# Optimization experiments

Hardware: AMD Instinct MI355X
Metric: run time of the kernel (lower is better)

Reference implementation:

```python
import jax, jax.numpy as jnp
import numpy as np

B, S, D = 4, 2048, 1024
H, HD = 16, 64  # num_heads, head_size
NEG = -1e20


def setup_inputs() -> dict:
    key = jax.random.key(0)
    ks = jax.random.split(key, 8)
    query = jax.random.normal(ks[0], (B, S, D), dtype=jnp.float32)
    k_in = jax.random.normal(ks[1], (B, S, D), dtype=jnp.float32)
    v_in = jax.random.normal(ks[2], (B, S, D), dtype=jnp.float32)
    # causal mask: True where attention is DISALLOWED (masked_fill semantics)
    mask = jnp.triu(jnp.ones((S, S), dtype=bool), k=1)
    scale = 1.0 / np.sqrt(D)
    Wq = jax.random.normal(ks[3], (D, H * HD), dtype=jnp.float32) * scale
    Wk = jax.random.normal(ks[4], (D, H * HD), dtype=jnp.float32) * scale
    Wv = jax.random.normal(ks[5], (D, H * HD), dtype=jnp.float32) * scale
    Wo = jax.random.normal(ks[6], (H * HD, D), dtype=jnp.float32) * scale
    bo = jnp.zeros((D,), dtype=jnp.float32)
    return {"query": query, "key": k_in, "value": v_in, "mask": mask,
            "Wq": Wq, "Wk": Wk, "Wv": Wv, "Wo": Wo, "bo": bo}


def reference(query, key, value, mask, Wq, Wk, Wv, Wo, bo):
    # projections -> [B, H, S, HD]
    q = (query @ Wq).reshape(B, -1, H, HD).transpose(0, 2, 1, 3)
    k = (key @ Wk).reshape(B, -1, H, HD).transpose(0, 2, 1, 3)
    v = (value @ Wv).reshape(B, -1, H, HD).transpose(0, 2, 1, 3)
    # scaled dot-product attention with boolean mask (True = masked out)
    scores = jnp.einsum('bhqd,bhkd->bhqk', q, k) / jnp.sqrt(jnp.float32(HD))
    scores = jnp.where(mask, jnp.float32(NEG), scores)
    attn = jax.nn.softmax(scores, axis=-1)
    out = jnp.einsum('bhqk,bhkd->bhqd', attn, v)  # [B,H,S,HD]
    out = out.transpose(0, 2, 1, 3).reshape(B, -1, H * HD)
    return out @ Wo + bo
```

## Files before the change

### kernel.cpp

```cpp
#include <hip/hip_runtime.h>

#define B_ 4
#define S_ 2048
#define D_ 1024
#define H_ 16
#define HD_ 64

typedef __attribute__((ext_vector_type(8))) short bf16x8;
typedef __attribute__((ext_vector_type(4))) float f32x4;

__device__ __forceinline__ short f2bf(float f) {
  unsigned u = __builtin_bit_cast(unsigned, f);
  u += 0x7fffu + ((u >> 16) & 1u);
  return (short)(u >> 16);
}

__device__ __forceinline__ unsigned cvtpk(float a, float b) {
  unsigned r;
  asm("v_cvt_pk_bf16_f32 %0, %1, %2" : "=v"(r) : "v"(a), "v"(b));
  return r;
}

__device__ __forceinline__ void gload_lds16(const void* g, void* l) {
  __builtin_amdgcn_global_load_lds((const __attribute__((address_space(1))) void*)g,
                                   (__attribute__((address_space(3))) void*)l, 16, 0, 0);
}

__device__ __forceinline__ bf16x8 ldsw8(const short* base, int row, int colb) {
  const int off = (row * 128 + colb) ^ ((row & 7) << 4);
  return *(const bf16x8*)((const char*)base + off);
}

#define MFMA16(a, b, c) __builtin_amdgcn_mfma_f32_16x16x32_bf16((a), (b), (c), 0, 0, 0)

__global__ void cast_f32_bf16(const float* __restrict__ in, short* __restrict__ out, int n4) {
  const int i = blockIdx.x * blockDim.x + threadIdx.x;
  if (i < n4) {
    const float4 f = ((const float4*)in)[i];
    short4 o;
    o.x = f2bf(f.x); o.y = f2bf(f.y); o.z = f2bf(f.z); o.w = f2bf(f.w);
    ((short4*)out)[i] = o;
  }
}

__global__ void transpose_cast_w4(const float* __restrict__ W0, const float* __restrict__ W1,
                                  const float* __restrict__ W2, const float* __restrict__ W3,
                                  short* __restrict__ T0, short* __restrict__ T1,
                                  short* __restrict__ T2, short* __restrict__ T3) {
  __shared__ float tile[32][33];
  const int z = blockIdx.z;
  const float* W = z == 0 ? W0 : z == 1 ? W1 : z == 2 ? W2 : W3;
  short* Wt = z == 0 ? T0 : z == 1 ? T1 : z == 2 ? T2 : T3;
  const int n0 = blockIdx.x * 32, k0 = blockIdx.y * 32;
  const int tx = threadIdx.x, ty = threadIdx.y;
  #pragma unroll
  for (int i = ty; i < 32; i += 8)
    tile[i][tx] = W[(size_t)(k0 + i) * 1024 + n0 + tx];
  __syncthreads();
  #pragma unroll
  for (int i = ty; i < 32; i += 8)
    Wt[(size_t)(n0 + i) * 1024 + k0 + tx] = f2bf(tile[tx][i]);
}

template <int LAYOUT>
__global__ __launch_bounds__(256) void gemm128(const short* __restrict__ A,
                                               const short* __restrict__ Bt,
                                               short* __restrict__ outb,
                                               float* __restrict__ outf,
                                               const float* __restrict__ bias,
                                               float oscale) {
  __shared__ __align__(16) short As[2][128 * 32];
  __shared__ __align__(16) short Bs[2][128 * 32];
  const int tid = threadIdx.x;
  const int l = tid & 63;
  const int w = tid >> 6;
  const int wm = w >> 1, wn = w & 1;
  const int flat = blockIdx.x + (blockIdx.y << 3);
  const int xcd = flat & 7, t = flat >> 3;
  const int row0 = (xcd * 8 + (t & 7)) * 128;
  const int col0 = (t >> 3) * 128;
  const int l15 = l & 15, lq = l >> 4;

  f32x4 acc[4][4] = {};

  auto stage = [&](const short* src, int r0, int k0, short* lds) {
    #pragma unroll
    for (int i = 0; i < 2; i++) {
      int eoff = w * 1024 + i * 512 + l * 8;
      int r = eoff >> 5, kk = eoff & 31;
      gload_lds16(src + (size_t)(r0 + r) * 1024 + k0 + kk, lds + w * 1024 + i * 512);
    }
  };

  stage(A, row0, 0, As[0]);
  stage(Bt, col0, 0, Bs[0]);

  for (int kt = 0; kt < 32; ++kt) {
    __syncthreads();
    if (kt + 1 < 32) {
      stage(A, row0, (kt + 1) * 32, As[(kt + 1) & 1]);
      stage(Bt, col0, (kt + 1) * 32, Bs[(kt + 1) & 1]);
    }
    const short* as = As[kt & 1];
    const short* bs = Bs[kt & 1];
    bf16x8 af[4], bfv[4];
    #pragma unroll
    for (int mf = 0; mf < 4; mf++)
      af[mf] = *(const bf16x8*)(as + (wm * 64 + mf * 16 + l15) * 32 + lq * 8);
    #pragma unroll
    for (int nf = 0; nf < 4; nf++)
      bfv[nf] = *(const bf16x8*)(bs + (wn * 64 + nf * 16 + l15) * 32 + lq * 8);
    #pragma unroll
    for (int mf = 0; mf < 4; mf++)
      #pragma unroll
      for (int nf = 0; nf < 4; nf++)
        acc[mf][nf] = MFMA16(af[mf], bfv[nf], acc[mf][nf]);
  }

  #pragma unroll
  for (int mf = 0; mf < 4; mf++) {
    #pragma unroll
    for (int nf = 0; nf < 4; nf++) {
      #pragma unroll
      for (int r = 0; r < 4; r++) {
        const int gr = row0 + wm * 64 + mf * 16 + lq * 4 + r;
        const int gc = col0 + wn * 64 + nf * 16 + l15;
        const float v = acc[mf][nf][r];
        if (LAYOUT == 0) {
          const int b = gr >> 11, s = gr & 2047;
          const int h = gc >> 6, hd = gc & 63;
          outb[(((size_t)(b * H_ + h)) * S_ + s) * HD_ + hd] = f2bf(v * oscale);
        } else if (LAYOUT == 1) {
          const int b = gr >> 11, s = gr & 2047;
          const int h = gc >> 6, hd = gc & 63;
          outb[(((size_t)(b * H_ + h)) * HD_ + hd) * S_ + s] = f2bf(v);
        } else {
          outf[(size_t)gr * 1024 + gc] = v + bias[gc];
        }
      }
    }
  }
}

__global__ __launch_bounds__(256) void attn_kernel(const short* __restrict__ Qh,
                                                   const short* __restrict__ Kh,
                                                   const short* __restrict__ Vtr,
                                                   short* __restrict__ attnout) {
  __shared__ __align__(16) short Ks[2][64 * 64];
  __shared__ __align__(16) short Vs[2][64 * 64];
  __shared__ __align__(16) short Ps[4][32 * 64];
  const int tid = threadIdx.x, l = tid & 63, w = tid >> 6;
  const int l15 = l & 15, lq = l >> 4;
  const int flat = blockIdx.x;
  const int vid = (flat & 7) * 64 + (flat >> 3);
  const int bh = vid >> 3, pairx = vid & 7;
  const int b = bh >> 4, h = bh & 15;
  const size_t base = (size_t)bh * (S_ * HD_);
  const short* Qp = Qh + base;
  const short* Kp = Kh + base;
  const short* Vp = Vtr + base;
  short* Pw = (short*)Ps[w];

  for (int pass = 0; pass < 2; ++pass) {
    const int qt = pass ? 15 - pairx : pairx;
    const int q0 = qt * 128;
    const int qw = q0 + w * 32;
    const int nkt = (q0 >> 6) + 2;

    bf16x8 qf[2][2];
    #pragma unroll
    for (int qh = 0; qh < 2; qh++)
      #pragma unroll
      for (int ks = 0; ks < 2; ks++)
        qf[qh][ks] = *(const bf16x8*)(Qp + (size_t)(qw + qh * 16 + l15) * 64 + ks * 32 + lq * 8);

    f32x4 oacc[4][2] = {};
    float mrow[2] = {-1e30f, -1e30f};
    float lpart[2] = {0.f, 0.f};

    auto stage = [&](int kt, int bf) {
      const int k0s = kt << 6;
      #pragma unroll
      for (int i = 0; i < 2; i++) {
        const int o = w * 2048 + i * 1024 + l * 16;
        const int sw = o ^ (((o >> 7) & 7) << 4);
        gload_lds16((const char*)Kp + (size_t)k0s * 128 + sw, (char*)Ks[bf] + o);
        gload_lds16(Vp + (size_t)(o >> 7) * S_ + k0s + ((sw & 127) >> 1), (char*)Vs[bf] + o);
      }
    };

    stage(0, 0);
    __syncthreads();

    for (int kt = 0; kt < nkt; ++kt) {
      const int cur = kt & 1;
      if (kt + 1 < nkt) stage(kt + 1, cur ^ 1);
      const int k0 = kt << 6;

      if (k0 <= qw + 31) {
        f32x4 sacc[2][4] = {};
        __builtin_amdgcn_s_setprio(1);
        #pragma unroll
        for (int ks = 0; ks < 2; ks++) {
          #pragma unroll
          for (int mf = 0; mf < 4; mf++) {
            const bf16x8 kf = ldsw8(Ks[cur], mf * 16 + l15, ks * 64 + lq * 16);
            #pragma unroll
            for (int qh = 0; qh < 2; qh++)
              sacc[qh][mf] = MFMA16(kf, qf[qh][ks], sacc[qh][mf]);
          }
        }
        __builtin_amdgcn_s_setprio(0);

        if (k0 + 63 > qw) {
          #pragma unroll
          for (int qh = 0; qh < 2; qh++) {
            const int qg = qw + qh * 16 + l15 - lq * 4;
            #pragma unroll
            for (int mf = 0; mf < 4; mf++)
              #pragma unroll
              for (int r = 0; r < 4; r++)
                if (k0 + mf * 16 + r > qg) sacc[qh][mf][r] = -1e30f;
          }
        }

        float mxl[2];
        #pragma unroll
        for (int qh = 0; qh < 2; qh++) {
          float m = fmaxf(fmaxf(sacc[qh][0][0], sacc[qh][0][1]),
                          fmaxf(sacc[qh][0][2], sacc[qh][0][3]));
          #pragma unroll
          for (int mf = 1; mf < 4; mf++)
            m = fmaxf(m, fmaxf(fmaxf(sacc[qh][mf][0], sacc[qh][mf][1]),
                               fmaxf(sacc[qh][mf][2], sacc[qh][mf][3])));
          mxl[qh] = m;
        }

        const bool need = (mxl[0] > mrow[0] + 8.f) || (mxl[1] > mrow[1] + 8.f);
        if (__any(need)) {
          #pragma unroll
          for (int qh = 0; qh < 2; qh++) {
            float m = fmaxf(mxl[qh], __shfl_xor(mxl[qh], 16));
            m = fmaxf(m, __shfl_xor(m, 32));
            const float mn = fmaxf(mrow[qh], m);
            const float fac = __builtin_amdgcn_exp2f(mrow[qh] - mn);
            mrow[qh] = mn;
            lpart[qh] *= fac;
            #pragma unroll
            for (int mf = 0; mf < 4; mf++) oacc[mf][qh] *= fac;
          }
        }

        #pragma unroll
        for (int qh = 0; qh < 2; qh++) {
          float rs = 0.f;
          const int row = qh * 16 + l15;
          #pragma unroll
          for (int mf = 0; mf < 4; mf++) {
            f32x4 p;
            #pragma unroll
            for (int r = 0; r < 4; r++) {
              const float e = __builtin_amdgcn_exp2f(sacc[qh][mf][r] - mrow[qh]);
              p[r] = e;
              rs += e;
            }
            const int off = (row * 128 + mf * 32 + lq * 8) ^ ((row & 7) << 4);
            *(uint2*)((char*)Pw + off) = make_uint2(cvtpk(p[0], p[1]), cvtpk(p[2], p[3]));
          }
          lpart[qh] += rs;
        }

        asm volatile("s_waitcnt lgkmcnt(0)" ::: "memory");
        __builtin_amdgcn_sched_barrier(0);

        __builtin_amdgcn_s_setprio(1);
        #pragma unroll
        for (int ks = 0; ks < 2; ks++) {
          bf16x8 pb[2];
          #pragma unroll
          for (int qh = 0; qh < 2; qh++) {
            const int row = qh * 16 + l15;
            const int off = (row * 128 + ks * 64 + lq * 16) ^ ((row & 7) << 4);
            pb[qh] = *(const bf16x8*)((const char*)Pw + off);
          }
          #pragma unroll
          for (int mf = 0; mf < 4; mf++) {
            const bf16x8 vf = ldsw8(Vs[cur], mf * 16 + l15, ks * 64 + lq * 16);
            #pragma unroll
            for (int qh = 0; qh < 2; qh++)
              oacc[mf][qh] = MFMA16(vf, pb[qh], oacc[mf][qh]);
          }
        }
        __builtin_amdgcn_s_setprio(0);
      }
      __syncthreads();
    }

    #pragma unroll
    for (int qh = 0; qh < 2; qh++) {
      float lr = lpart[qh];
      lr += __shfl_xor(lr, 16);
      lr += __shfl_xor(lr, 32);
      const float rinv = __builtin_amdgcn_rcpf(lr);
      const int q = qw + qh * 16 + l15;
      #pragma unroll
      for (int mf = 0; mf < 4; mf++) {
        const f32x4 o = oacc[mf][qh];
        const uint2 u = make_uint2(cvtpk(o[0] * rinv, o[1] * rinv),
                                   cvtpk(o[2] * rinv, o[3] * rinv));
        *(uint2*)(attnout + ((size_t)b * S_ + q) * (H_ * HD_) + h * 64 + mf * 16 + lq * 4) = u;
      }
    }
  }
}

extern "C" void kernel_launch(void* const* d_in, const int* in_sizes, int n_in,
                              void* d_out, int out_size, void* d_ws, size_t ws_size,
                              hipStream_t stream) {
  const float* query = (const float*)d_in[0];
  const float* key_  = (const float*)d_in[1];
  const float* value = (const float*)d_in[2];
  const float* Wq = (const float*)d_in[4];
  const float* Wk = (const float*)d_in[5];
  const float* Wv = (const float*)d_in[6];
  const float* Wo = (const float*)d_in[7];
  const float* bo = (const float*)d_in[8];
  float* out = (float*)d_out;

  char* ws = (char*)d_ws;
  const size_t MB = (size_t)1 << 20;
  short* Xbuf = (short*)(ws);
  short* Wqt  = (short*)(ws + 16 * MB);
  short* Wkt  = (short*)(ws + 18 * MB);
  short* Wvt  = (short*)(ws + 20 * MB);
  short* Wot  = (short*)(ws + 22 * MB);
  short* Qh   = (short*)(ws + 24 * MB);
  short* Kh   = (short*)(ws + 40 * MB);
  short* Vt   = (short*)(ws + 56 * MB);

  const int NE = B_ * S_ * D_;
  const int n4 = NE / 4;
  const dim3 tb(32, 8);
  const dim3 tg4(32, 32, 4);
  const dim3 gb(8, 64);
  const float QSCALE = 0.125f * 1.4426950408889634f;

  transpose_cast_w4<<<tg4, tb, 0, stream>>>(Wq, Wk, Wv, Wo, Wqt, Wkt, Wvt, Wot);

  cast_f32_bf16<<<n4 / 256, 256, 0, stream>>>(query, Xbuf, n4);
  gemm128<0><<<gb, 256, 0, stream>>>(Xbuf, Wqt, Qh, nullptr, nullptr, QSCALE);
  cast_f32_bf16<<<n4 / 256, 256, 0, stream>>>(key_, Xbuf, n4);
  gemm128<0><<<gb, 256, 0, stream>>>(Xbuf, Wkt, Kh, nullptr, nullptr, 1.0f);
  cast_f32_bf16<<<n4 / 256, 256, 0, stream>>>(value, Xbuf, n4);
  gemm128<1><<<gb, 256, 0, stream>>>(Xbuf, Wvt, Vt, nullptr, nullptr, 1.0f);

  attn_kernel<<<dim3(512), 256, 0, stream>>>(Qh, Kh, Vt, Xbuf);

  gemm128<2><<<gb, 256, 0, stream>>>(Xbuf, Wot, nullptr, out, bo, 1.0f);
}
```

Before: 227.9 us.

## Fuse fp32-to-bf16 input cast into a batched QKV projection GEMM

Removes the three separate cast kernels and instead loads fp32 activations straight into LDS with a swizzled layout, converting them to bf16 in registers just before the MFMA. The three Q/K/V projection GEMMs are merged into one launch over a z dimension, which cuts launch count and fills more CUs at once. In exchange the A tile in LDS doubles in size (fp32), so each k-step moves more LDS and global bytes and does extra conversion work inside the inner loop, and LDS use per block rises, which can lower occupancy.

```diff
diff --git a/kernel.cpp b/kernel.cpp
--- a/kernel.cpp
+++ b/kernel.cpp
@@ -8,6 +8,7 @@
 
 typedef __attribute__((ext_vector_type(8))) short bf16x8;
 typedef __attribute__((ext_vector_type(4))) float f32x4;
+typedef __attribute__((ext_vector_type(4))) unsigned u32x4;
 
 __device__ __forceinline__ short f2bf(float f) {
   unsigned u = __builtin_bit_cast(unsigned, f);
@@ -32,16 +33,6 @@
 }
 
 #define MFMA16(a, b, c) __builtin_amdgcn_mfma_f32_16x16x32_bf16((a), (b), (c), 0, 0, 0)
-
-__global__ void cast_f32_bf16(const float* __restrict__ in, short* __restrict__ out, int n4) {
-  const int i = blockIdx.x * blockDim.x + threadIdx.x;
-  if (i < n4) {
-    const float4 f = ((const float4*)in)[i];
-    short4 o;
-    o.x = f2bf(f.x); o.y = f2bf(f.y); o.z = f2bf(f.z); o.w = f2bf(f.w);
-    ((short4*)out)[i] = o;
-  }
-}
 
 __global__ void transpose_cast_w4(const float* __restrict__ W0, const float* __restrict__ W1,
                                   const float* __restrict__ W2, const float* __restrict__ W3,
@@ -62,13 +53,111 @@
     Wt[(size_t)(n0 + i) * 1024 + k0 + tx] = f2bf(tile[tx][i]);
 }
 
-template <int LAYOUT>
-__global__ __launch_bounds__(256) void gemm128(const short* __restrict__ A,
-                                               const short* __restrict__ Bt,
-                                               short* __restrict__ outb,
-                                               float* __restrict__ outf,
-                                               const float* __restrict__ bias,
-                                               float oscale) {
+__global__ __launch_bounds__(256) void gemm_qkv(const float* __restrict__ Aq,
+                                                const float* __restrict__ Ak,
+                                                const float* __restrict__ Av,
+                                                const short* __restrict__ Bq,
+                                                const short* __restrict__ Bk,
+                                                const short* __restrict__ Bv,
+                                                short* __restrict__ Oq,
+                                                short* __restrict__ Ok,
+                                                short* __restrict__ Ov,
+                                                float qscale) {
+  __shared__ __align__(16) float Asf[2][128 * 32];
+  __shared__ __align__(16) short Bs[2][128 * 32];
+  const int z = blockIdx.z;
+  const float* A = z == 0 ? Aq : z == 1 ? Ak : Av;
+  const short* Bt = z == 0 ? Bq : z == 1 ? Bk : Bv;
+  short* outb = z == 0 ? Oq : z == 1 ? Ok : Ov;
+  const float oscale = z == 0 ? qscale : 1.0f;
+
+  const int tid = threadIdx.x;
+  const int l = tid & 63, w = tid >> 6;
+  const int wm = w >> 1, wn = w & 1;
+  const int flat = blockIdx.x + (blockIdx.y << 3);
+  const int xcd = flat & 7, t = flat >> 3;
+  const int row0 = (xcd * 8 + (t & 7)) * 128;
+  const int col0 = (t >> 3) * 128;
+  const int l15 = l & 15, lq = l >> 4;
+
+  f32x4 acc[4][4] = {};
+
+  auto stageA = [&](int k0, int buf) {
+    #pragma unroll
+    for (int i = 0; i < 4; i++) {
+      const int eoff = w * 4096 + i * 1024 + l * 16;
+      const int row = eoff >> 7;
+      const int sc = (eoff & 127) ^ ((row & 7) << 4);
+      gload_lds16((const char*)A + (size_t)(row0 + row) * 4096 + (size_t)k0 * 4 + sc,
+                  (char*)Asf[buf] + w * 4096 + i * 1024);
+    }
+  };
+  auto stageB = [&](int k0, int buf) {
+    #pragma unroll
+    for (int i = 0; i < 2; i++) {
+      const int eoff = w * 1024 + i * 512 + l * 8;
+      const int r = eoff >> 5, kk = eoff & 31;
+      gload_lds16(Bt + (size_t)(col0 + r) * 1024 + k0 + kk,
+                  (short*)Bs[buf] + w * 1024 + i * 512);
+    }
+  };
+
+  stageA(0, 0);
+  stageB(0, 0);
+
+  for (int kt = 0; kt < 32; ++kt) {
+    __syncthreads();
+    if (kt + 1 < 32) {
+      stageA((kt + 1) * 32, (kt + 1) & 1);
+      stageB((kt + 1) * 32, (kt + 1) & 1);
+    }
+    const float* as = Asf[kt & 1];
+    const short* bs = Bs[kt & 1];
+    bf16x8 af[4], bfv[4];
+    #pragma unroll
+    for (int mf = 0; mf < 4; mf++) {
+      const int R = wm * 64 + mf * 16 + l15;
+      const int sw = (R & 7) << 4;
+      const f32x4 g0 = *(const f32x4*)((const char*)as + R * 128 + ((lq * 32) ^ sw));
+      const f32x4 g1 = *(const f32x4*)((const char*)as + R * 128 + ((lq * 32 + 16) ^ sw));
+      const u32x4 uu = {cvtpk(g0[0], g0[1]), cvtpk(g0[2], g0[3]),
+                        cvtpk(g1[0], g1[1]), cvtpk(g1[2], g1[3])};
+      af[mf] = __builtin_bit_cast(bf16x8, uu);
+    }
+    #pragma unroll
+    for (int nf = 0; nf < 4; nf++)
+      bfv[nf] = *(const bf16x8*)(bs + (wn * 64 + nf * 16 + l15) * 32 + lq * 8);
+    #pragma unroll
+    for (int mf = 0; mf < 4; mf++)
+      #pragma unroll
+      for (int nf = 0; nf < 4; nf++)
+        acc[mf][nf] = MFMA16(af[mf], bfv[nf], acc[mf][nf]);
+  }
+
+  #pragma unroll
+  for (int mf = 0; mf < 4; mf++) {
+    #pragma unroll
+    for (int nf = 0; nf < 4; nf++) {
+      #pragma unroll
+      for (int r = 0; r < 4; r++) {
+        const int gr = row0 + wm * 64 + mf * 16 + lq * 4 + r;
+        const int gc = col0 + wn * 64 + nf * 16 + l15;
+        const int b = gr >> 11, s = gr & 2047;
+        const int h = gc >> 6, hd = gc & 63;
+        const float v = acc[mf][nf][r];
+        if (z < 2)
+          outb[(((size_t)(b * H_ + h)) * S_ + s) * HD_ + hd] = f2bf(v * oscale);
+        else
+          outb[(((size_t)(b * H_ + h)) * HD_ + hd) * S_ + s] = f2bf(v);
+      }
+    }
+  }
+}
+
+__global__ __launch_bounds__(256) void gemm_o(const short* __restrict__ A,
+                                              const short* __restrict__ Bt,
+                                              float* __restrict__ outf,
+                                              const float* __restrict__ bias) {
   __shared__ __align__(16) short As[2][128 * 32];
   __shared__ __align__(16) short Bs[2][128 * 32];
   const int tid = threadIdx.x;
@@ -118,28 +207,15 @@
   }
 
   #pragma unroll
-  for (int mf = 0; mf < 4; mf++) {
-    #pragma unroll
-    for (int nf = 0; nf < 4; nf++) {
+  for (int mf = 0; mf < 4; mf++)
+    #pragma unroll
+    for (int nf = 0; nf < 4; nf++)
       #pragma unroll
       for (int r = 0; r < 4; r++) {
         const int gr = row0 + wm * 64 + mf * 16 + lq * 4 + r;
         const int gc = col0 + wn * 64 + nf * 16 + l15;
-        const float v = acc[mf][nf][r];
-        if (LAYOUT == 0) {
-          const int b = gr >> 11, s = gr & 2047;
-          const int h = gc >> 6, hd = gc & 63;
-          outb[(((size_t)(b * H_ + h)) * S_ + s) * HD_ + hd] = f2bf(v * oscale);
-        } else if (LAYOUT == 1) {
-          const int b = gr >> 11, s = gr & 2047;
-          const int h = gc >> 6, hd = gc & 63;
-          outb[(((size_t)(b * H_ + h)) * HD_ + hd) * S_ + s] = f2bf(v);
-        } else {
-          outf[(size_t)gr * 1024 + gc] = v + bias[gc];
-        }
+        outf[(size_t)gr * 1024 + gc] = acc[mf][nf][r] + bias[gc];
       }
-    }
-  }
 }
 
 __global__ __launch_bounds__(256) void attn_kernel(const short* __restrict__ Qh,
@@ -338,23 +414,17 @@
   short* Kh   = (short*)(ws + 40 * MB);
   short* Vt   = (short*)(ws + 56 * MB);
 
-  const int NE = B_ * S_ * D_;
-  const int n4 = NE / 4;
   const dim3 tb(32, 8);
   const dim3 tg4(32, 32, 4);
-  const dim3 gb(8, 64);
   const float QSCALE = 0.125f * 1.4426950408889634f;
 
   transpose_cast_w4<<<tg4, tb, 0, stream>>>(Wq, Wk, Wv, Wo, Wqt, Wkt, Wvt, Wot);
 
-  cast_f32_bf16<<<n4 / 256, 256, 0, stream>>>(query, Xbuf, n4);
-  gemm128<0><<<gb, 256, 0, stream>>>(Xbuf, Wqt, Qh, nullptr, nullptr, QSCALE);
-  cast_f32_bf16<<<n4 / 256, 256, 0, stream>>>(key_, Xbuf, n4);
-  gemm128<0><<<gb, 256, 0, stream>>>(Xbuf, Wkt, Kh, nullptr, nullptr, 1.0f);
-  cast_f32_bf16<<<n4 / 256, 256, 0, stream>>>(value, Xbuf, n4);
-  gemm128<1><<<gb, 256, 0, stream>>>(Xbuf, Wvt, Vt, nullptr, nullptr, 1.0f);
+  gemm_qkv<<<dim3(8, 64, 3), 256, 0, stream>>>(query, key_, value,
+                                               Wqt, Wkt, Wvt,
+                                               Qh, Kh, Vt, QSCALE);
 
   attn_kernel<<<dim3(512), 256, 0, stream>>>(Qh, Kh, Vt, Xbuf);
 
-  gemm128<2><<<gb, 256, 0, stream>>>(Xbuf, Wot, nullptr, out, bo, 1.0f);
-}
+  gemm_o<<<dim3(8, 64), 256, 0, stream>>>(Xbuf, Wot, out, bo);
+}
```

After: 200.5 us. -12.0%, faster.

## Batch QKV projections into one 256x256-tile pipelined GEMM launch

Applied to the files above, without the earlier changes.

Replaces the 128x128 GEMM with a 256x256-tile, 512-thread kernel that uses a K-step of 64, a swizzled LDS layout, and staggered global-to-LDS prefetch interleaved with MFMA phases under explicit waitcnt and barriers. The three Q/K/V casts become one launch, and the three projections become one launch indexed by blockIdx.z, so three serial small launches are gone and more blocks are in flight. The goal is better data reuse and overlap of loads with matrix math. The cost is more LDS and registers per block, fragile hand-tuned waitcnt ordering, and more workspace for the three separate bf16 input copies.

```diff
diff --git a/kernel.cpp b/kernel.cpp
--- a/kernel.cpp
+++ b/kernel.cpp
@@ -32,16 +32,9 @@
 }
 
 #define MFMA16(a, b, c) __builtin_amdgcn_mfma_f32_16x16x32_bf16((a), (b), (c), 0, 0, 0)
-
-__global__ void cast_f32_bf16(const float* __restrict__ in, short* __restrict__ out, int n4) {
-  const int i = blockIdx.x * blockDim.x + threadIdx.x;
-  if (i < n4) {
-    const float4 f = ((const float4*)in)[i];
-    short4 o;
-    o.x = f2bf(f.x); o.y = f2bf(f.y); o.z = f2bf(f.z); o.w = f2bf(f.w);
-    ((short4*)out)[i] = o;
-  }
-}
+#define PBAR()   asm volatile("s_barrier" ::: "memory")
+#define LGKM0()  do { asm volatile("s_waitcnt lgkmcnt(0)" ::: "memory"); \
+                      __builtin_amdgcn_sched_barrier(0); } while (0)
 
 __global__ void transpose_cast_w4(const float* __restrict__ W0, const float* __restrict__ W1,
                                   const float* __restrict__ W2, const float* __restrict__ W3,
@@ -62,78 +55,126 @@
     Wt[(size_t)(n0 + i) * 1024 + k0 + tx] = f2bf(tile[tx][i]);
 }
 
-template <int LAYOUT>
-__global__ __launch_bounds__(256) void gemm128(const short* __restrict__ A,
-                                               const short* __restrict__ Bt,
-                                               short* __restrict__ outb,
-                                               float* __restrict__ outf,
-                                               const float* __restrict__ bias,
-                                               float oscale) {
-  __shared__ __align__(16) short As[2][128 * 32];
-  __shared__ __align__(16) short Bs[2][128 * 32];
+__global__ void cast3(const float* __restrict__ q, const float* __restrict__ k,
+                      const float* __restrict__ v, short* __restrict__ oq,
+                      short* __restrict__ ok, short* __restrict__ ov) {
+  const int z = blockIdx.z;
+  const float* in = z == 0 ? q : z == 1 ? k : v;
+  short* out = z == 0 ? oq : z == 1 ? ok : ov;
+  const int i = blockIdx.x * 256 + threadIdx.x;
+  const float4 f = ((const float4*)in)[i];
+  ((uint2*)out)[i] = make_uint2(cvtpk(f.x, f.y), cvtpk(f.z, f.w));
+}
+
+template <int MODE>
+__global__ __launch_bounds__(512, 2) void gemm8(const short* __restrict__ A0p,
+                                                const short* __restrict__ A1p,
+                                                const short* __restrict__ A2p,
+                                                const short* __restrict__ Bt0,
+                                                const short* __restrict__ Bt1,
+                                                const short* __restrict__ Bt2,
+                                                short* __restrict__ O0,
+                                                short* __restrict__ O1,
+                                                short* __restrict__ O2,
+                                                float* __restrict__ outf,
+                                                const float* __restrict__ bias,
+                                                float qscale) {
+  __shared__ __align__(16) short lds[2][4][8192];
+  const int z = (MODE == 0) ? blockIdx.z : 0;
+  const short* A = z == 0 ? A0p : z == 1 ? A1p : A2p;
+  const short* Bt = z == 0 ? Bt0 : z == 1 ? Bt1 : Bt2;
+  short* outb = z == 0 ? O0 : z == 1 ? O1 : O2;
+  const float oscale = (MODE == 0 && z == 0) ? qscale : 1.0f;
+
   const int tid = threadIdx.x;
-  const int l = tid & 63;
-  const int w = tid >> 6;
-  const int wm = w >> 1, wn = w & 1;
-  const int flat = blockIdx.x + (blockIdx.y << 3);
-  const int xcd = flat & 7, t = flat >> 3;
-  const int row0 = (xcd * 8 + (t & 7)) * 128;
-  const int col0 = (t >> 3) * 128;
+  const int l = tid & 63, w = tid >> 6;
+  const int wm = w >> 2, wn = w & 3;
   const int l15 = l & 15, lq = l >> 4;
-
-  f32x4 acc[4][4] = {};
-
-  auto stage = [&](const short* src, int r0, int k0, short* lds) {
+  const int flat = blockIdx.x + (blockIdx.y << 2);
+  const int vid = (flat & 7) * 16 + (flat >> 3);
+  const int row0 = (vid >> 2) * 256;
+  const int col0 = (vid & 3) * 256;
+
+  f32x4 acc[8][4] = {};
+
+  auto stageH = [&](short* dst, const short* src, int rbase, int hrow, int kt) {
     #pragma unroll
-    for (int i = 0; i < 2; i++) {
-      int eoff = w * 1024 + i * 512 + l * 8;
-      int r = eoff >> 5, kk = eoff & 31;
-      gload_lds16(src + (size_t)(r0 + r) * 1024 + k0 + kk, lds + w * 1024 + i * 512);
+    for (int j = 0; j < 2; ++j) {
+      const int o2 = w * 1024 + j * 8192 + l * 16;
+      const int row = o2 >> 7;
+      const int sc = (o2 & 127) ^ ((row & 7) << 4);
+      gload_lds16((const char*)src + ((size_t)(rbase + hrow + row) * 1024 + kt * 64) * 2 + sc,
+                  (char*)dst + o2);
     }
   };
 
-  stage(A, row0, 0, As[0]);
-  stage(Bt, col0, 0, Bs[0]);
-
-  for (int kt = 0; kt < 32; ++kt) {
-    __syncthreads();
-    if (kt + 1 < 32) {
-      stage(A, row0, (kt + 1) * 32, As[(kt + 1) & 1]);
-      stage(Bt, col0, (kt + 1) * 32, Bs[(kt + 1) & 1]);
+  stageH(lds[0][2], Bt, col0, 0, 0);
+  stageH(lds[0][3], Bt, col0, 128, 0);
+  stageH(lds[0][0], A, row0, 0, 0);
+  stageH(lds[0][1], A, row0, 128, 0);
+  stageH(lds[1][2], Bt, col0, 0, 1);
+  stageH(lds[1][3], Bt, col0, 128, 1);
+
+  for (int t = 0; t < 16; ++t) {
+    const int c = t & 1, o = c ^ 1;
+    if (t < 15) asm volatile("s_waitcnt vmcnt(4)" ::: "memory");
+    else        asm volatile("s_waitcnt vmcnt(0)" ::: "memory");
+    PBAR();
+
+    const short* Ah = lds[c][wm];
+    const short* Bh = lds[c][2 + (wn >> 1)];
+    const int brow = (wn & 1) * 64;
+    bf16x8 bfr[4][2];
+
+    #pragma unroll
+    for (int p = 0; p < 4; ++p) {
+      if (p == 0 && t + 1 < 16) stageH(lds[o][0], A, row0, 0, t + 1);
+      if (p == 1 && t + 1 < 16) stageH(lds[o][1], A, row0, 128, t + 1);
+      if (p == 1 && t + 2 < 16) stageH(lds[c][2], Bt, col0, 0, t + 2);
+      if (p == 2 && t + 2 < 16) stageH(lds[c][3], Bt, col0, 128, t + 2);
+
+      if (p == 0) {
+        #pragma unroll
+        for (int nf = 0; nf < 4; ++nf)
+          #pragma unroll
+          for (int ks = 0; ks < 2; ++ks)
+            bfr[nf][ks] = ldsw8(Bh, brow + nf * 16 + l15, ks * 64 + lq * 16);
+      }
+      const bf16x8 a00 = ldsw8(Ah, (2 * p) * 16 + l15, lq * 16);
+      const bf16x8 a01 = ldsw8(Ah, (2 * p) * 16 + l15, 64 + lq * 16);
+      const bf16x8 a10 = ldsw8(Ah, (2 * p + 1) * 16 + l15, lq * 16);
+      const bf16x8 a11 = ldsw8(Ah, (2 * p + 1) * 16 + l15, 64 + lq * 16);
+
+      LGKM0();
+      __builtin_amdgcn_s_setprio(1);
+      #pragma unroll
+      for (int nf = 0; nf < 4; ++nf) {
+        acc[2 * p][nf]     = MFMA16(a00, bfr[nf][0], acc[2 * p][nf]);
+        acc[2 * p][nf]     = MFMA16(a01, bfr[nf][1], acc[2 * p][nf]);
+        acc[2 * p + 1][nf] = MFMA16(a10, bfr[nf][0], acc[2 * p + 1][nf]);
+        acc[2 * p + 1][nf] = MFMA16(a11, bfr[nf][1], acc[2 * p + 1][nf]);
+      }
+      __builtin_amdgcn_s_setprio(0);
+      PBAR();
     }
-    const short* as = As[kt & 1];
-    const short* bs = Bs[kt & 1];
-    bf16x8 af[4], bfv[4];
+  }
+
+  #pragma unroll
+  for (int mf = 0; mf < 8; ++mf) {
     #pragma unroll
-    for (int mf = 0; mf < 4; mf++)
-      af[mf] = *(const bf16x8*)(as + (wm * 64 + mf * 16 + l15) * 32 + lq * 8);
-    #pragma unroll
-    for (int nf = 0; nf < 4; nf++)
-      bfv[nf] = *(const bf16x8*)(bs + (wn * 64 + nf * 16 + l15) * 32 + lq * 8);
-    #pragma unroll
-    for (int mf = 0; mf < 4; mf++)
+    for (int nf = 0; nf < 4; ++nf) {
       #pragma unroll
-      for (int nf = 0; nf < 4; nf++)
-        acc[mf][nf] = MFMA16(af[mf], bfv[nf], acc[mf][nf]);
-  }
-
-  #pragma unroll
-  for (int mf = 0; mf < 4; mf++) {
-    #pragma unroll
-    for (int nf = 0; nf < 4; nf++) {
-      #pragma unroll
-      for (int r = 0; r < 4; r++) {
-        const int gr = row0 + wm * 64 + mf * 16 + lq * 4 + r;
+      for (int r = 0; r < 4; ++r) {
+        const int gr = row0 + wm * 128 + mf * 16 + lq * 4 + r;
         const int gc = col0 + wn * 64 + nf * 16 + l15;
         const float v = acc[mf][nf][r];
-        if (LAYOUT == 0) {
+        if (MODE == 0) {
           const int b = gr >> 11, s = gr & 2047;
           const int h = gc >> 6, hd = gc & 63;
-          outb[(((size_t)(b * H_ + h)) * S_ + s) * HD_ + hd] = f2bf(v * oscale);
-        } else if (LAYOUT == 1) {
-          const int b = gr >> 11, s = gr & 2047;
-          const int h = gc >> 6, hd = gc & 63;
-          outb[(((size_t)(b * H_ + h)) * HD_ + hd) * S_ + s] = f2bf(v);
+          if (z < 2)
+            outb[(((size_t)(b * H_ + h)) * S_ + s) * HD_ + hd] = f2bf(v * oscale);
+          else
+            outb[(((size_t)(b * H_ + h)) * HD_ + hd) * S_ + s] = f2bf(v);
         } else {
           outf[(size_t)gr * 1024 + gc] = v + bias[gc];
         }
@@ -329,32 +370,31 @@
 
   char* ws = (char*)d_ws;
   const size_t MB = (size_t)1 << 20;
+  short* Aq   = (short*)(ws);
+  short* Ak   = (short*)(ws + 16 * MB);
+  short* Av   = (short*)(ws + 32 * MB);
   short* Xbuf = (short*)(ws);
-  short* Wqt  = (short*)(ws + 16 * MB);
-  short* Wkt  = (short*)(ws + 18 * MB);
-  short* Wvt  = (short*)(ws + 20 * MB);
-  short* Wot  = (short*)(ws + 22 * MB);
-  short* Qh   = (short*)(ws + 24 * MB);
-  short* Kh   = (short*)(ws + 40 * MB);
-  short* Vt   = (short*)(ws + 56 * MB);
-
-  const int NE = B_ * S_ * D_;
-  const int n4 = NE / 4;
+  short* Wqt  = (short*)(ws + 48 * MB);
+  short* Wkt  = (short*)(ws + 50 * MB);
+  short* Wvt  = (short*)(ws + 52 * MB);
+  short* Wot  = (short*)(ws + 54 * MB);
+  short* Qh   = (short*)(ws + 56 * MB);
+  short* Kh   = (short*)(ws + 72 * MB);
+  short* Vt   = (short*)(ws + 88 * MB);
+
   const dim3 tb(32, 8);
   const dim3 tg4(32, 32, 4);
-  const dim3 gb(8, 64);
   const float QSCALE = 0.125f * 1.4426950408889634f;
 
   transpose_cast_w4<<<tg4, tb, 0, stream>>>(Wq, Wk, Wv, Wo, Wqt, Wkt, Wvt, Wot);
 
-  cast_f32_bf16<<<n4 / 256, 256, 0, stream>>>(query, Xbuf, n4);
-  gemm128<0><<<gb, 256, 0, stream>>>(Xbuf, Wqt, Qh, nullptr, nullptr, QSCALE);
-  cast_f32_bf16<<<n4 / 256, 256, 0, stream>>>(key_, Xbuf, n4);
-  gemm128<0><<<gb, 256, 0, stream>>>(Xbuf, Wkt, Kh, nullptr, nullptr, 1.0f);
-  cast_f32_bf16<<<n4 / 256, 256, 0, stream>>>(value, Xbuf, n4);
-  gemm128<1><<<gb, 256, 0, stream>>>(Xbuf, Wvt, Vt, nullptr, nullptr, 1.0f);
+  cast3<<<dim3(8192, 1, 3), 256, 0, stream>>>(query, key_, value, Aq, Ak, Av);
+
+  gemm8<0><<<dim3(4, 32, 3), 512, 0, stream>>>(Aq, Ak, Av, Wqt, Wkt, Wvt,
+                                               Qh, Kh, Vt, nullptr, nullptr, QSCALE);
 
   attn_kernel<<<dim3(512), 256, 0, stream>>>(Qh, Kh, Vt, Xbuf);
 
-  gemm128<2><<<gb, 256, 0, stream>>>(Xbuf, Wot, nullptr, out, bo, 1.0f);
-}
+  gemm8<1><<<dim3(4, 32, 1), 512, 0, stream>>>(Xbuf, nullptr, nullptr, Wot, nullptr, nullptr,
+                                               nullptr, nullptr, nullptr, out, bo, 1.0f);
+}
```

Measured after the change: 220.5 us. 3.3% less time.
